# Performance work log

Hardware: AMD Instinct MI355X
Metric: run time of the kernel (lower is better)

## Reference

```python
import jax, jax.numpy as jnp
import numpy as np

B, S, H, NH = 2, 2048, 1024, 16
HD = H // NH
INV_NORM = 1.0 / float(np.sqrt(HD))
BETA = 1.0


def setup_inputs() -> dict:
    key = jax.random.key(0)
    ks = jax.random.split(key, 8)
    causal = ~jnp.tril(jnp.ones((S, S), dtype=bool))  # True = masked (future)
    return {
        "hidden_states": jax.random.normal(ks[0], (B, S, H), dtype=jnp.float32),
        "residual": jax.random.normal(ks[1], (B, S, H), dtype=jnp.float32),
        "alibi": jax.random.normal(ks[2], (B * NH, 1, S), dtype=jnp.float32) * 0.1,
        "attention_mask": jnp.broadcast_to(causal[None, None], (B, 1, S, S)),
        "W_qkv": jax.random.normal(ks[3], (3 * H, H), dtype=jnp.float32) * (1.0 / np.sqrt(H)),
        "b_qkv": jax.random.normal(ks[4], (3 * H,), dtype=jnp.float32) * 0.02,
        "W_d": jax.random.normal(ks[5], (H, H), dtype=jnp.float32) * (1.0 / np.sqrt(H)),
        "b_d": jax.random.normal(ks[6], (H,), dtype=jnp.float32) * 0.02,
    }


def reference(hidden_states, residual, alibi, attention_mask, W_qkv, b_qkv, W_d, b_d):
    b, s, h = hidden_states.shape
    # fused QKV projection, split per-head interleaved [B,S,NH,3,HD]
    fused = hidden_states @ W_qkv.T + b_qkv
    fused = fused.reshape(b, s, NH, 3, HD)
    q = jnp.transpose(fused[..., 0, :], (0, 2, 1, 3))  # [B,NH,S,HD]
    k = jnp.transpose(fused[..., 1, :], (0, 2, 1, 3))
    v = jnp.transpose(fused[..., 2, :], (0, 2, 1, 3))
    # baddbmm: beta*alibi + alpha * q @ k^T
    scores = BETA * alibi.reshape(b, NH, 1, s) + INV_NORM * jnp.einsum(
        "bhqd,bhkd->bhqk", q, k
    )  # [B,NH,S,S]
    neg_min = jnp.finfo(scores.dtype).min
    scores = jnp.where(attention_mask, neg_min, scores)
    probs = jax.nn.softmax(scores.astype(jnp.float32), axis=-1).astype(scores.dtype)
    ctx = jnp.einsum("bhqk,bhkd->bhqd", probs, v)  # [B,NH,S,HD]
    ctx = jnp.transpose(ctx, (0, 2, 1, 3)).reshape(b, s, h)  # merge heads
    out = ctx @ W_d.T + b_d
    return residual + out  # dropout p=0
```

## Files before the change

kernel.cpp:

```cpp
#include <hip/hip_runtime.h>
#include <stdint.h>

#define BATCH 2
#define SLEN 2048
#define HDIM 1024
#define NH 16
#define HD 64
#define NHEADS 32
#define M_ROWS 4096
#define N_QKV 3072

typedef float f32x4 __attribute__((ext_vector_type(4)));
typedef float f32x16 __attribute__((ext_vector_type(16)));
typedef short bf16x8 __attribute__((ext_vector_type(8)));

typedef __attribute__((address_space(1))) unsigned int GU32;
typedef __attribute__((address_space(3))) unsigned int LU32;

__device__ __forceinline__ void gld16(const void* g, void* l) {
  __builtin_amdgcn_global_load_lds((GU32*)g, (LU32*)l, 16, 0, 0);
}

__device__ __forceinline__ unsigned short f2bf(float x) {
  union { float f; unsigned int u; } v; v.f = x;
  unsigned int r = v.u + 0x7fffu + ((v.u >> 16) & 1u);
  return (unsigned short)(r >> 16);
}

__device__ __forceinline__ float fexp2(float x) {
  float r; asm("v_exp_f32 %0, %1" : "=v"(r) : "v"(x)); return r;
}
__device__ __forceinline__ unsigned cvtpk(float lo, float hi) {
  unsigned r; asm("v_cvt_pk_bf16_f32 %0, %1, %2" : "=v"(r) : "v"(lo), "v"(hi)); return r;
}

#define MFMA32(a, b, c) __builtin_amdgcn_mfma_f32_32x32x16_bf16(a, b, c, 0, 0, 0)
#define MFMA16(a, b, c) __builtin_amdgcn_mfma_f32_16x16x32_bf16(a, b, c, 0, 0, 0)
#define ZERO16 {0.f,0.f,0.f,0.f,0.f,0.f,0.f,0.f,0.f,0.f,0.f,0.f,0.f,0.f,0.f,0.f}

__global__ void __launch_bounds__(256) k_prep(
    const float* __restrict__ hidden, const float* __restrict__ wqkv,
    const float* __restrict__ wd,
    unsigned short* __restrict__ hb, unsigned short* __restrict__ wqkb,
    unsigned short* __restrict__ wdb) {
  int bid = blockIdx.x;
  const float* src;
  unsigned short* dst;
  int i;
  if (bid < 4096)      { src = hidden; dst = hb;   i = bid * 256 + threadIdx.x; }
  else if (bid < 7168) { src = wqkv;  dst = wqkb;  i = (bid - 4096) * 256 + threadIdx.x; }
  else                 { src = wd;    dst = wdb;   i = (bid - 7168) * 256 + threadIdx.x; }
  float4 v = ((const float4*)src)[i];
  ushort4 o;
  o.x = f2bf(v.x); o.y = f2bf(v.y); o.z = f2bf(v.z); o.w = f2bf(v.w);
  ((ushort4*)dst)[i] = o;
}

__global__ void __launch_bounds__(256) k_gemm_qkv(
    const unsigned short* __restrict__ A,
    const unsigned short* __restrict__ Bw,
    const float* __restrict__ bias,
    unsigned short* __restrict__ Qo,
    unsigned short* __restrict__ Ko,
    unsigned short* __restrict__ Vto) {
  __shared__ __align__(16) unsigned short Alds[128 * 32];
  __shared__ __align__(16) unsigned short Blds[128 * 32];
  const int tid = threadIdx.x;
  const int w = tid >> 6, lane = tid & 63;
  const int g = lane >> 4, l15 = lane & 15;
  const int wr = w >> 1, wc = w & 1;
  const int tm = blockIdx.x * 128, tn = blockIdx.y * 128;

  const f32x4 zero = {0.f, 0.f, 0.f, 0.f};
  f32x4 acc[4][4];
#pragma unroll
  for (int m = 0; m < 4; ++m)
#pragma unroll
    for (int n = 0; n < 4; ++n) acc[m][n] = zero;

  for (int k0 = 0; k0 < 1024; k0 += 32) {
    __syncthreads();
#pragma unroll
    for (int r = 0; r < 2; ++r) {
      int c = r * 256 + w * 64 + lane;
      int row = c >> 2, cc = c & 3;
      gld16(A + (size_t)(tm + row) * 1024 + k0 + cc * 8,
            (char*)Alds + (r * 256 + w * 64) * 16);
      gld16(Bw + (size_t)(tn + row) * 1024 + k0 + cc * 8,
            (char*)Blds + (r * 256 + w * 64) * 16);
    }
    __syncthreads();
    bf16x8 af[4], bfv[4];
#pragma unroll
    for (int m = 0; m < 4; ++m)
      af[m] = *(const bf16x8*)(Alds + (wr * 64 + m * 16 + l15) * 32 + g * 8);
#pragma unroll
    for (int n = 0; n < 4; ++n)
      bfv[n] = *(const bf16x8*)(Blds + (wc * 64 + n * 16 + l15) * 32 + g * 8);
#pragma unroll
    for (int m = 0; m < 4; ++m)
#pragma unroll
      for (int n = 0; n < 4; ++n)
        acc[m][n] = MFMA16(af[m], bfv[n], acc[m][n]);
  }

#pragma unroll
  for (int n = 0; n < 4; ++n) {
    int col = tn + wc * 64 + n * 16 + l15;
    float bv = bias[col];
    int c6 = col >> 6;
    int nh = c6 / 3;
    int which = c6 - nh * 3;
    int hd = col & 63;
#pragma unroll
    for (int m = 0; m < 4; ++m) {
      int row0 = tm + wr * 64 + m * 16 + g * 4;
      int b = row0 >> 11;
      int s0 = row0 & 2047;
      int head = b * NH + nh;
      if (which == 2) {
        ushort4 pk;
        pk.x = f2bf(acc[m][n][0] + bv);
        pk.y = f2bf(acc[m][n][1] + bv);
        pk.z = f2bf(acc[m][n][2] + bv);
        pk.w = f2bf(acc[m][n][3] + bv);
        *(ushort4*)(Vto + ((size_t)head * HD + hd) * SLEN + s0) = pk;
      } else {
        unsigned short* dst = (which == 0) ? Qo : Ko;
        size_t base = (size_t)head * SLEN * HD;
#pragma unroll
        for (int j = 0; j < 4; ++j)
          dst[base + (size_t)(s0 + j) * HD + hd] = f2bf(acc[m][n][j] + bv);
      }
    }
  }
}

__global__ void __launch_bounds__(256) k_gemm_out(
    const unsigned short* __restrict__ A,
    const unsigned short* __restrict__ Bw,
    const float* __restrict__ bias,
    const float* __restrict__ residual,
    float* __restrict__ out) {
  __shared__ __align__(16) unsigned short Alds[128 * 32];
  __shared__ __align__(16) unsigned short Blds[64 * 32];
  const int tid = threadIdx.x;
  const int w = tid >> 6, lane = tid & 63;
  const int g = lane >> 4, l15 = lane & 15;
  const int wr = w >> 1, wc = w & 1;
  const int tm = blockIdx.x * 128, tn = blockIdx.y * 64;

  const f32x4 zero = {0.f, 0.f, 0.f, 0.f};
  f32x4 acc[4][2];
#pragma unroll
  for (int m = 0; m < 4; ++m)
#pragma unroll
    for (int n = 0; n < 2; ++n) acc[m][n] = zero;

  for (int k0 = 0; k0 < 1024; k0 += 32) {
    __syncthreads();
#pragma unroll
    for (int r = 0; r < 2; ++r) {
      int c = r * 256 + tid;
      int row = c >> 2, cc = c & 3;
      gld16(A + (size_t)(tm + row) * 1024 + k0 + cc * 8,
            (char*)Alds + c * 16);
    }
    {
      int row = tid >> 2, cc = tid & 3;
      gld16(Bw + (size_t)(tn + row) * 1024 + k0 + cc * 8,
            (char*)Blds + tid * 16);
    }
    __syncthreads();
    bf16x8 af[4], bfv[2];
#pragma unroll
    for (int m = 0; m < 4; ++m)
      af[m] = *(const bf16x8*)(Alds + (wr * 64 + m * 16 + l15) * 32 + g * 8);
#pragma unroll
    for (int n = 0; n < 2; ++n)
      bfv[n] = *(const bf16x8*)(Blds + (wc * 32 + n * 16 + l15) * 32 + g * 8);
#pragma unroll
    for (int m = 0; m < 4; ++m)
#pragma unroll
      for (int n = 0; n < 2; ++n)
        acc[m][n] = MFMA16(af[m], bfv[n], acc[m][n]);
  }

#pragma unroll
  for (int n = 0; n < 2; ++n) {
    int col = tn + wc * 32 + n * 16 + l15;
    float bv = bias[col];
#pragma unroll
    for (int m = 0; m < 4; ++m) {
      int row0 = tm + wr * 64 + m * 16 + g * 4;
#pragma unroll
      for (int j = 0; j < 4; ++j) {
        size_t idx = (size_t)(row0 + j) * 1024 + col;
        out[idx] = acc[m][n][j] + bv + residual[idx];
      }
    }
  }
}

__global__ void __launch_bounds__(512, 4) k_attn(
    const unsigned short* __restrict__ Q,
    const unsigned short* __restrict__ K,
    const unsigned short* __restrict__ Vt,
    const float* __restrict__ alibi,
    unsigned short* __restrict__ ctx) {
  __shared__ __align__(16) char Lbuf[40960];
  unsigned short* KlB = (unsigned short*)Lbuf;
  unsigned short* VlB = (unsigned short*)(Lbuf + 16384);
  float* Al = (float*)(Lbuf + 32768);

  const int n = blockIdx.x;
  const int head = n & 31;
  const int t = n >> 5;
  const int bq = (t < 8) ? (15 - t) : (t - 8);
  const int tid = threadIdx.x;
  const int w = tid >> 6, lane = tid & 63;
  const int l31 = lane & 31, h = lane >> 5;
  const int rsw = l31 & 7;
  const int qsub = w & 3, par = w >> 2;
  const int qw = bq * 128 + qsub * 32;
  const int ksd = 4 * bq + qsub;

  const unsigned short* Qh = Q + (size_t)head * SLEN * HD;
  const unsigned short* Kh = K + (size_t)head * SLEN * HD;
  const unsigned short* Vh = Vt + (size_t)head * HD * SLEN;

  bf16x8 qr0, qr1, qr2, qr3;
  {
    const unsigned short* qp = Qh + (size_t)(qw + l31) * HD + h * 8;
    qr0 = *(const bf16x8*)(qp);
    qr1 = *(const bf16x8*)(qp + 16);
    qr2 = *(const bf16x8*)(qp + 32);
    qr3 = *(const bf16x8*)(qp + 48);
  }

  f32x16 ot0 = ZERO16, ot1 = ZERO16;
  float m_run = -1e30f, l_acc = 0.f;
  const float C1 = 0.18033688011f;

#define STAGE(nb, itt)                                                          \
  do {                                                                          \
    const int kb_ = (itt) * 64;                                                 \
    const int row_ = tid >> 3;                                                  \
    const int sw_ = ((tid & 7) ^ (row_ & 7)) * 8;                               \
    gld16(Kh + (size_t)(kb_ + row_) * HD + sw_, (char*)(KlB + (nb) * 4096) + tid * 16); \
    gld16(Vh + (size_t)row_ * SLEN + kb_ + sw_, (char*)(VlB + (nb) * 4096) + tid * 16); \
  } while (0)

  STAGE(0, 0);
  {
    float4 av = *(const float4*)(alibi + (size_t)head * SLEN + tid * 4);
    av.x *= 1.44269504f; av.y *= 1.44269504f;
    av.z *= 1.44269504f; av.w *= 1.44269504f;
    *(float4*)(Al + tid * 4) = av;
  }
  __syncthreads();
  int cur = 0;
  const int itmax = 2 * bq + 2;

  for (int it = 0; it < itmax; ++it) {
    if (it + 1 < itmax) STAGE(cur ^ 1, it + 1);
    const int ks = 2 * it + par;
    if (ks <= ksd) {
      const char* kbase = (const char*)(KlB + cur * 4096);
      const char* vbase = (const char*)(VlB + cur * 4096);

      f32x16 st = ZERO16;
      __builtin_amdgcn_s_setprio(1);
      {
        const char* kr = kbase + (par * 32 + l31) * 128;
        st = MFMA32(*(const bf16x8*)(kr + (((0 + h) ^ rsw) * 16)), qr0, st);
        st = MFMA32(*(const bf16x8*)(kr + (((2 + h) ^ rsw) * 16)), qr1, st);
        st = MFMA32(*(const bf16x8*)(kr + (((4 + h) ^ rsw) * 16)), qr2, st);
        st = MFMA32(*(const bf16x8*)(kr + (((6 + h) ^ rsw) * 16)), qr3, st);
      }
      __builtin_amdgcn_s_setprio(0);

      const float* ab = Al + ks * 32 + 4 * h;
      f32x4 alq0 = *(const f32x4*)(ab);
      f32x4 alq1 = *(const f32x4*)(ab + 8);
      f32x4 alq2 = *(const f32x4*)(ab + 16);
      f32x4 alq3 = *(const f32x4*)(ab + 24);

      float p[16];
#pragma unroll
      for (int i = 0; i < 4; ++i) {
        p[i]      = st[i]      * C1 + alq0[i];
        p[4 + i]  = st[4 + i]  * C1 + alq1[i];
        p[8 + i]  = st[8 + i]  * C1 + alq2[i];
        p[12 + i] = st[12 + i] * C1 + alq3[i];
      }
      if (ks == ksd) {
#pragma unroll
        for (int i = 0; i < 16; ++i) {
          int krow = (i & 3) + 8 * (i >> 2) + 4 * h;
          p[i] = (krow > l31) ? -1e30f : p[i];
        }
      }
      float x0 = fmaxf(fmaxf(p[0], p[1]), p[2]);
      float x1 = fmaxf(fmaxf(p[3], p[4]), p[5]);
      float x2 = fmaxf(fmaxf(p[6], p[7]), p[8]);
      float x3 = fmaxf(fmaxf(p[9], p[10]), p[11]);
      float x4 = fmaxf(fmaxf(p[12], p[13]), p[14]);
      float pm = fmaxf(fmaxf(fmaxf(x0, x1), x2), fmaxf(fmaxf(x3, x4), p[15]));
      pm = fmaxf(pm, __shfl_xor(pm, 32));
      if (!__all(pm <= m_run + 8.0f)) {
        float mnew = fmaxf(m_run, pm);
        float sc = fexp2(m_run - mnew);
        m_run = mnew;
        l_acc *= sc;
        ot0 *= sc;
        ot1 *= sc;
      }
      float e[16];
      float ss = 0.f;
#pragma unroll
      for (int i = 0; i < 16; ++i) { e[i] = fexp2(p[i] - m_run); ss += e[i]; }
      l_acc += ss;

      unsigned a0 = cvtpk(e[0], e[1]),   a1 = cvtpk(e[2], e[3]);
      unsigned a2 = cvtpk(e[4], e[5]),   a3 = cvtpk(e[6], e[7]);
      unsigned b0 = cvtpk(e[8], e[9]),   b1 = cvtpk(e[10], e[11]);
      unsigned b2 = cvtpk(e[12], e[13]), b3 = cvtpk(e[14], e[15]);
      unsigned t0 = h ? a0 : a2, t1 = h ? a1 : a3;
      unsigned t2 = h ? b0 : b2, t3 = h ? b1 : b3;
      unsigned r0 = __shfl_xor(t0, 32), r1 = __shfl_xor(t1, 32);
      unsigned r2 = __shfl_xor(t2, 32), r3 = __shfl_xor(t3, 32);
      union { unsigned u[4]; bf16x8 v; } P0, P1;
      P0.u[0] = h ? r0 : a0;  P0.u[1] = h ? r1 : a1;
      P0.u[2] = h ? a2 : r0;  P0.u[3] = h ? a3 : r1;
      P1.u[0] = h ? r2 : b0;  P1.u[1] = h ? r3 : b1;
      P1.u[2] = h ? b2 : r2;  P1.u[3] = h ? b3 : r3;

      __builtin_amdgcn_s_setprio(1);
      {
        const char* vr0 = vbase + l31 * 128;
        const char* vr1 = vbase + (32 + l31) * 128;
        bf16x8 vf;
        vf = *(const bf16x8*)(vr0 + (((4 * par + 0 + h) ^ rsw) * 16)); ot0 = MFMA32(vf, P0.v, ot0);
        vf = *(const bf16x8*)(vr0 + (((4 * par + 2 + h) ^ rsw) * 16)); ot0 = MFMA32(vf, P1.v, ot0);
        vf = *(const bf16x8*)(vr1 + (((4 * par + 0 + h) ^ rsw) * 16)); ot1 = MFMA32(vf, P0.v, ot1);
        vf = *(const bf16x8*)(vr1 + (((4 * par + 2 + h) ^ rsw) * 16)); ot1 = MFMA32(vf, P1.v, ot1);
      }
      __builtin_amdgcn_s_setprio(0);
    }
    __syncthreads();
    cur ^= 1;
  }
#undef STAGE

  float* Ob = (float*)Lbuf;
  float* Mb = (float*)(Lbuf + 32768);
  const int idx = qsub * 64 + lane;
  const int xs = idx & 7;
  float* op = Ob + (size_t)idx * 32;
  if (par == 1) {
#pragma unroll
    for (int c = 0; c < 4; ++c) {
      f32x4 t2 = {ot0[4 * c], ot0[4 * c + 1], ot0[4 * c + 2], ot0[4 * c + 3]};
      *(f32x4*)(op + ((c ^ xs) * 4)) = t2;
      f32x4 u = {ot1[4 * c], ot1[4 * c + 1], ot1[4 * c + 2], ot1[4 * c + 3]};
      *(f32x4*)(op + (((c + 4) ^ xs) * 4)) = u;
    }
    Mb[idx * 2] = m_run;
    Mb[idx * 2 + 1] = l_acc;
  }
  __syncthreads();
  if (par == 0) {
    float m1 = Mb[idx * 2], l1 = Mb[idx * 2 + 1];
    float mt = fmaxf(m_run, m1);
    float s0 = fexp2(m_run - mt), s1 = fexp2(m1 - mt);
    float lme = l_acc * s0 + l1 * s1;
    float ltot = lme + __shfl_xor(lme, 32);
    float inv = 1.0f / ltot;
#pragma unroll
    for (int c = 0; c < 4; ++c) {
      f32x4 t2 = *(const f32x4*)(op + ((c ^ xs) * 4));
      f32x4 u = *(const f32x4*)(op + (((c + 4) ^ xs) * 4));
#pragma unroll
      for (int j = 0; j < 4; ++j) {
        ot0[4 * c + j] = ot0[4 * c + j] * s0 + t2[j] * s1;
        ot1[4 * c + j] = ot1[4 * c + j] * s0 + u[j] * s1;
      }
    }
    const int b = head >> 4, nh = head & 15;
    unsigned short* cb = ctx + ((size_t)b * SLEN + qw + l31) * HDIM + nh * HD + 4 * h;
#pragma unroll
    for (int rg = 0; rg < 4; ++rg) {
      ushort4 o;
      o.x = f2bf(ot0[4 * rg + 0] * inv);
      o.y = f2bf(ot0[4 * rg + 1] * inv);
      o.z = f2bf(ot0[4 * rg + 2] * inv);
      o.w = f2bf(ot0[4 * rg + 3] * inv);
      *(ushort4*)(cb + 8 * rg) = o;
      o.x = f2bf(ot1[4 * rg + 0] * inv);
      o.y = f2bf(ot1[4 * rg + 1] * inv);
      o.z = f2bf(ot1[4 * rg + 2] * inv);
      o.w = f2bf(ot1[4 * rg + 3] * inv);
      *(ushort4*)(cb + 32 + 8 * rg) = o;
    }
  }
}

extern "C" void kernel_launch(void* const* d_in, const int* in_sizes, int n_in,
                              void* d_out, int out_size, void* d_ws, size_t ws_size,
                              hipStream_t stream) {
  const float* hidden   = (const float*)d_in[0];
  const float* residual = (const float*)d_in[1];
  const float* alibi    = (const float*)d_in[2];
  const float* W_qkv = (const float*)d_in[4];
  const float* b_qkv = (const float*)d_in[5];
  const float* W_d   = (const float*)d_in[6];
  const float* b_d   = (const float*)d_in[7];
  float* out = (float*)d_out;

  unsigned short* hb   = (unsigned short*)d_ws;
  unsigned short* wqkb = hb + (size_t)M_ROWS * HDIM;
  unsigned short* wdb  = wqkb + (size_t)N_QKV * HDIM;
  unsigned short* Qb   = wdb + (size_t)HDIM * HDIM;
  unsigned short* Kb   = Qb + (size_t)NHEADS * SLEN * HD;
  unsigned short* Vtb  = Kb + (size_t)NHEADS * SLEN * HD;
  unsigned short* ctxb = Vtb + (size_t)NHEADS * SLEN * HD;

  k_prep<<<dim3(8192), dim3(256), 0, stream>>>(hidden, W_qkv, W_d, hb, wqkb, wdb);
  k_gemm_qkv<<<dim3(32, 24), dim3(256), 0, stream>>>(hb, wqkb, b_qkv, Qb, Kb, Vtb);
  k_attn<<<dim3(512), dim3(512), 0, stream>>>(Qb, Kb, Vtb, alibi, ctxb);
  k_gemm_out<<<dim3(32, 16), dim3(256), 0, stream>>>(ctxb, wdb, b_d, residual, out);
}
```

Measured before the change: 103.0 us.

## Split attention blocks to 64 query rows with 4-way KV split and single-buffered 128-key tiles

The attention kernel now gives each block 64 query rows instead of 128 and launches twice as many blocks. Four warp groups now split the key range instead of two, followed by a two-stage LDS merge of the partial softmax states. Each iteration stages a 128-key K/V tile into a single buffer with a new 16-way V swizzle, in place of the double-buffered 64-key pipeline. The aim is more parallelism and better balance across the causal triangle. The cost is that load/compute overlap is lost, since a barrier now follows each stage, and the merge phase adds extra barriers.

Measured after the change: 104.5 us. Within noise of the previous version (+1.5%).

```diff
diff --git a/kernel.cpp b/kernel.cpp
--- a/kernel.cpp
+++ b/kernel.cpp
@@ -213,17 +213,17 @@
   unsigned short* VlB = (unsigned short*)(Lbuf + 16384);
   float* Al = (float*)(Lbuf + 32768);
 
-  const int n = blockIdx.x;
-  const int head = n & 31;
-  const int t = n >> 5;
-  const int bq = (t < 8) ? (15 - t) : (t - 8);
+  const int bid = blockIdx.x;
+  const int head = bid & 31;
+  const int bq = 31 - (bid >> 5);
   const int tid = threadIdx.x;
   const int w = tid >> 6, lane = tid & 63;
   const int l31 = lane & 31, h = lane >> 5;
   const int rsw = l31 & 7;
-  const int qsub = w & 3, par = w >> 2;
-  const int qw = bq * 128 + qsub * 32;
-  const int ksd = 4 * bq + qsub;
+  const int vsw = l31 & 15;
+  const int qsub = w & 1, par = w >> 1;
+  const int qw = bq * 64 + qsub * 32;
+  const int ksd = 2 * bq + qsub;
 
   const unsigned short* Qh = Q + (size_t)head * SLEN * HD;
   const unsigned short* Kh = K + (size_t)head * SLEN * HD;
@@ -242,37 +242,39 @@
   float m_run = -1e30f, l_acc = 0.f;
   const float C1 = 0.18033688011f;
 
-#define STAGE(nb, itt)                                                          \
-  do {                                                                          \
-    const int kb_ = (itt) * 64;                                                 \
-    const int row_ = tid >> 3;                                                  \
-    const int sw_ = ((tid & 7) ^ (row_ & 7)) * 8;                               \
-    gld16(Kh + (size_t)(kb_ + row_) * HD + sw_, (char*)(KlB + (nb) * 4096) + tid * 16); \
-    gld16(Vh + (size_t)row_ * SLEN + kb_ + sw_, (char*)(VlB + (nb) * 4096) + tid * 16); \
+#define STAGE(itt)                                                                  \
+  do {                                                                              \
+    const int kb_ = (itt) * 128;                                                    \
+    const int r0_ = tid >> 3, c0_ = tid & 7;                                        \
+    gld16(Kh + (size_t)(kb_ + r0_) * HD + ((c0_ ^ (r0_ & 7)) * 8),                  \
+          (char*)KlB + tid * 16);                                                   \
+    gld16(Kh + (size_t)(kb_ + 64 + r0_) * HD + ((c0_ ^ (r0_ & 7)) * 8),             \
+          (char*)KlB + (512 + tid) * 16);                                           \
+    const int vr0_ = tid >> 4, vc0_ = tid & 15;                                     \
+    gld16(Vh + (size_t)vr0_ * SLEN + kb_ + ((vc0_ ^ (vr0_ & 15)) * 8),              \
+          (char*)VlB + tid * 16);                                                   \
+    gld16(Vh + (size_t)(32 + vr0_) * SLEN + kb_ + ((vc0_ ^ (vr0_ & 15)) * 8),       \
+          (char*)VlB + (512 + tid) * 16);                                           \
   } while (0)
 
-  STAGE(0, 0);
   {
     float4 av = *(const float4*)(alibi + (size_t)head * SLEN + tid * 4);
     av.x *= 1.44269504f; av.y *= 1.44269504f;
     av.z *= 1.44269504f; av.w *= 1.44269504f;
     *(float4*)(Al + tid * 4) = av;
   }
-  __syncthreads();
-  int cur = 0;
-  const int itmax = 2 * bq + 2;
+
+  const int itmax = (2 * bq + 1) / 4 + 1;
 
   for (int it = 0; it < itmax; ++it) {
-    if (it + 1 < itmax) STAGE(cur ^ 1, it + 1);
-    const int ks = 2 * it + par;
+    STAGE(it);
+    __syncthreads();
+    const int ks = 4 * it + par;
     if (ks <= ksd) {
-      const char* kbase = (const char*)(KlB + cur * 4096);
-      const char* vbase = (const char*)(VlB + cur * 4096);
-
       f32x16 st = ZERO16;
       __builtin_amdgcn_s_setprio(1);
       {
-        const char* kr = kbase + (par * 32 + l31) * 128;
+        const char* kr = (const char*)KlB + (par * 32 + l31) * 128;
         st = MFMA32(*(const bf16x8*)(kr + (((0 + h) ^ rsw) * 16)), qr0, st);
         st = MFMA32(*(const bf16x8*)(kr + (((2 + h) ^ rsw) * 16)), qr1, st);
         st = MFMA32(*(const bf16x8*)(kr + (((4 + h) ^ rsw) * 16)), qr2, st);
@@ -338,55 +340,69 @@
 
       __builtin_amdgcn_s_setprio(1);
       {
-        const char* vr0 = vbase + l31 * 128;
-        const char* vr1 = vbase + (32 + l31) * 128;
+        const char* vr0 = (const char*)VlB + l31 * 256;
+        const char* vr1 = (const char*)VlB + (32 + l31) * 256;
         bf16x8 vf;
-        vf = *(const bf16x8*)(vr0 + (((4 * par + 0 + h) ^ rsw) * 16)); ot0 = MFMA32(vf, P0.v, ot0);
-        vf = *(const bf16x8*)(vr0 + (((4 * par + 2 + h) ^ rsw) * 16)); ot0 = MFMA32(vf, P1.v, ot0);
-        vf = *(const bf16x8*)(vr1 + (((4 * par + 0 + h) ^ rsw) * 16)); ot1 = MFMA32(vf, P0.v, ot1);
-        vf = *(const bf16x8*)(vr1 + (((4 * par + 2 + h) ^ rsw) * 16)); ot1 = MFMA32(vf, P1.v, ot1);
+        vf = *(const bf16x8*)(vr0 + (((4 * par + 0 + h) ^ vsw) * 16)); ot0 = MFMA32(vf, P0.v, ot0);
+        vf = *(const bf16x8*)(vr0 + (((4 * par + 2 + h) ^ vsw) * 16)); ot0 = MFMA32(vf, P1.v, ot0);
+        vf = *(const bf16x8*)(vr1 + (((4 * par + 0 + h) ^ vsw) * 16)); ot1 = MFMA32(vf, P0.v, ot1);
+        vf = *(const bf16x8*)(vr1 + (((4 * par + 2 + h) ^ vsw) * 16)); ot1 = MFMA32(vf, P1.v, ot1);
       }
       __builtin_amdgcn_s_setprio(0);
     }
     __syncthreads();
-    cur ^= 1;
   }
 #undef STAGE
 
   float* Ob = (float*)Lbuf;
   float* Mb = (float*)(Lbuf + 32768);
-  const int idx = qsub * 64 + lane;
-  const int xs = idx & 7;
-  float* op = Ob + (size_t)idx * 32;
-  if (par == 1) {
-#pragma unroll
-    for (int c = 0; c < 4; ++c) {
-      f32x4 t2 = {ot0[4 * c], ot0[4 * c + 1], ot0[4 * c + 2], ot0[4 * c + 3]};
-      *(f32x4*)(op + ((c ^ xs) * 4)) = t2;
-      f32x4 u = {ot1[4 * c], ot1[4 * c + 1], ot1[4 * c + 2], ot1[4 * c + 3]};
-      *(f32x4*)(op + (((c + 4) ^ xs) * 4)) = u;
-    }
-    Mb[idx * 2] = m_run;
-    Mb[idx * 2 + 1] = l_acc;
-  }
+  const int xs = lane & 7;
+
+#define WRITE_SLOT(slot)                                                   \
+  do {                                                                     \
+    float* op = Ob + ((size_t)(slot) * 64 + lane) * 32;                    \
+    _Pragma("unroll")                                                      \
+    for (int c = 0; c < 4; ++c) {                                          \
+      f32x4 t2 = {ot0[4*c], ot0[4*c+1], ot0[4*c+2], ot0[4*c+3]};           \
+      *(f32x4*)(op + ((c ^ xs) * 4)) = t2;                                 \
+      f32x4 u2 = {ot1[4*c], ot1[4*c+1], ot1[4*c+2], ot1[4*c+3]};           \
+      *(f32x4*)(op + (((c + 4) ^ xs) * 4)) = u2;                           \
+    }                                                                      \
+    Mb[((slot) * 64 + lane) * 2] = m_run;                                  \
+    Mb[((slot) * 64 + lane) * 2 + 1] = l_acc;                              \
+  } while (0)
+
+#define MERGE_SLOT(slot)                                                   \
+  do {                                                                     \
+    const float* op = Ob + ((size_t)(slot) * 64 + lane) * 32;              \
+    float m1 = Mb[((slot) * 64 + lane) * 2];                               \
+    float l1 = Mb[((slot) * 64 + lane) * 2 + 1];                           \
+    float mt = fmaxf(m_run, m1);                                           \
+    float s0 = fexp2(m_run - mt), s1 = fexp2(m1 - mt);                     \
+    m_run = mt;                                                            \
+    l_acc = l_acc * s0 + l1 * s1;                                          \
+    _Pragma("unroll")                                                      \
+    for (int c = 0; c < 4; ++c) {                                          \
+      f32x4 t2 = *(const f32x4*)(op + ((c ^ xs) * 4));                     \
+      f32x4 u2 = *(const f32x4*)(op + (((c + 4) ^ xs) * 4));               \
+      _Pragma("unroll")                                                    \
+      for (int j = 0; j < 4; ++j) {                                        \
+        ot0[4*c+j] = ot0[4*c+j] * s0 + t2[j] * s1;                         \
+        ot1[4*c+j] = ot1[4*c+j] * s0 + u2[j] * s1;                         \
+      }                                                                    \
+    }                                                                      \
+  } while (0)
+
+  if (par == 1 || par == 3) WRITE_SLOT(qsub * 2 + (par >> 1));
+  __syncthreads();
+  if (par == 0 || par == 2) MERGE_SLOT(qsub * 2 + (par >> 1));
+  __syncthreads();
+  if (par == 2) WRITE_SLOT(qsub * 2);
   __syncthreads();
   if (par == 0) {
-    float m1 = Mb[idx * 2], l1 = Mb[idx * 2 + 1];
-    float mt = fmaxf(m_run, m1);
-    float s0 = fexp2(m_run - mt), s1 = fexp2(m1 - mt);
-    float lme = l_acc * s0 + l1 * s1;
-    float ltot = lme + __shfl_xor(lme, 32);
+    MERGE_SLOT(qsub * 2);
+    float ltot = l_acc + __shfl_xor(l_acc, 32);
     float inv = 1.0f / ltot;
-#pragma unroll
-    for (int c = 0; c < 4; ++c) {
-      f32x4 t2 = *(const f32x4*)(op + ((c ^ xs) * 4));
-      f32x4 u = *(const f32x4*)(op + (((c + 4) ^ xs) * 4));
-#pragma unroll
-      for (int j = 0; j < 4; ++j) {
-        ot0[4 * c + j] = ot0[4 * c + j] * s0 + t2[j] * s1;
-        ot1[4 * c + j] = ot1[4 * c + j] * s0 + u[j] * s1;
-      }
-    }
     const int b = head >> 4, nh = head & 15;
     unsigned short* cb = ctx + ((size_t)b * SLEN + qw + l31) * HDIM + nh * HD + 4 * h;
 #pragma unroll
@@ -404,6 +420,8 @@
       *(ushort4*)(cb + 32 + 8 * rg) = o;
     }
   }
+#undef WRITE_SLOT
+#undef MERGE_SLOT
 }
 
 extern "C" void kernel_launch(void* const* d_in, const int* in_sizes, int n_in,
@@ -428,6 +446,6 @@
 
   k_prep<<<dim3(8192), dim3(256), 0, stream>>>(hidden, W_qkv, W_d, hb, wqkb, wdb);
   k_gemm_qkv<<<dim3(32, 24), dim3(256), 0, stream>>>(hb, wqkb, b_qkv, Qb, Kb, Vtb);
-  k_attn<<<dim3(512), dim3(512), 0, stream>>>(Qb, Kb, Vtb, alibi, ctxb);
+  k_attn<<<dim3(1024), dim3(512), 0, stream>>>(Qb, Kb, Vtb, alibi, ctxb);
   k_gemm_out<<<dim3(32, 16), dim3(256), 0, stream>>>(ctxb, wdb, b_d, residual, out);
 }
```

## Load K/V fragments directly from global memory in attention, drop LDS staging

Applied to the files above, without the earlier changes.

The attention kernel stops staging K and V tiles into shared memory with double-buffered global_load_lds and block-wide barriers. Each wave now reads its own K and V fragments straight from global memory (relying on L2/L1 for reuse) and iterates only its own key steps, with no per-iteration __syncthreads. The alibi prescale by log2(e) moves into the prep kernel, and attention reads the scaled alibi from global memory instead of LDS. This removes barrier coupling between waves, but loses the shared reuse of K/V across the four query sub-waves and exposes global load latency without explicit prefetch.

New measurement: 138.9 us. 34.9% more time.

```diff
diff --git a/kernel.cpp b/kernel.cpp
--- a/kernel.cpp
+++ b/kernel.cpp
@@ -40,16 +40,23 @@
 
 __global__ void __launch_bounds__(256) k_prep(
     const float* __restrict__ hidden, const float* __restrict__ wqkv,
-    const float* __restrict__ wd,
+    const float* __restrict__ wd, const float* __restrict__ alibi,
     unsigned short* __restrict__ hb, unsigned short* __restrict__ wqkb,
-    unsigned short* __restrict__ wdb) {
+    unsigned short* __restrict__ wdb, float* __restrict__ al2) {
   int bid = blockIdx.x;
   const float* src;
   unsigned short* dst;
   int i;
   if (bid < 4096)      { src = hidden; dst = hb;   i = bid * 256 + threadIdx.x; }
   else if (bid < 7168) { src = wqkv;  dst = wqkb;  i = (bid - 4096) * 256 + threadIdx.x; }
-  else                 { src = wd;    dst = wdb;   i = (bid - 7168) * 256 + threadIdx.x; }
+  else if (bid < 8192) { src = wd;    dst = wdb;   i = (bid - 7168) * 256 + threadIdx.x; }
+  else {
+    int j = (bid - 8192) * 256 + threadIdx.x;
+    float4 v = ((const float4*)alibi)[j];
+    v.x *= 1.44269504f; v.y *= 1.44269504f; v.z *= 1.44269504f; v.w *= 1.44269504f;
+    ((float4*)al2)[j] = v;
+    return;
+  }
   float4 v = ((const float4*)src)[i];
   ushort4 o;
   o.x = f2bf(v.x); o.y = f2bf(v.y); o.z = f2bf(v.z); o.w = f2bf(v.w);
@@ -206,12 +213,10 @@
     const unsigned short* __restrict__ Q,
     const unsigned short* __restrict__ K,
     const unsigned short* __restrict__ Vt,
-    const float* __restrict__ alibi,
+    const float* __restrict__ al2,
     unsigned short* __restrict__ ctx) {
-  __shared__ __align__(16) char Lbuf[40960];
-  unsigned short* KlB = (unsigned short*)Lbuf;
-  unsigned short* VlB = (unsigned short*)(Lbuf + 16384);
-  float* Al = (float*)(Lbuf + 32768);
+  __shared__ __align__(16) float Ob[256 * 32];
+  __shared__ __align__(16) float Mb[256 * 2];
 
   const int n = blockIdx.x;
   const int head = n & 31;
@@ -220,7 +225,6 @@
   const int tid = threadIdx.x;
   const int w = tid >> 6, lane = tid & 63;
   const int l31 = lane & 31, h = lane >> 5;
-  const int rsw = l31 & 7;
   const int qsub = w & 3, par = w >> 2;
   const int qw = bq * 128 + qsub * 32;
   const int ksd = 4 * bq + qsub;
@@ -228,6 +232,7 @@
   const unsigned short* Qh = Q + (size_t)head * SLEN * HD;
   const unsigned short* Kh = K + (size_t)head * SLEN * HD;
   const unsigned short* Vh = Vt + (size_t)head * HD * SLEN;
+  const float* alh = al2 + (size_t)head * SLEN;
 
   bf16x8 qr0, qr1, qr2, qr3;
   {
@@ -242,119 +247,98 @@
   float m_run = -1e30f, l_acc = 0.f;
   const float C1 = 0.18033688011f;
 
-#define STAGE(nb, itt)                                                          \
-  do {                                                                          \
-    const int kb_ = (itt) * 64;                                                 \
-    const int row_ = tid >> 3;                                                  \
-    const int sw_ = ((tid & 7) ^ (row_ & 7)) * 8;                               \
-    gld16(Kh + (size_t)(kb_ + row_) * HD + sw_, (char*)(KlB + (nb) * 4096) + tid * 16); \
-    gld16(Vh + (size_t)row_ * SLEN + kb_ + sw_, (char*)(VlB + (nb) * 4096) + tid * 16); \
-  } while (0)
-
-  STAGE(0, 0);
-  {
-    float4 av = *(const float4*)(alibi + (size_t)head * SLEN + tid * 4);
-    av.x *= 1.44269504f; av.y *= 1.44269504f;
-    av.z *= 1.44269504f; av.w *= 1.44269504f;
-    *(float4*)(Al + tid * 4) = av;
-  }
-  __syncthreads();
-  int cur = 0;
-  const int itmax = 2 * bq + 2;
-
-  for (int it = 0; it < itmax; ++it) {
-    if (it + 1 < itmax) STAGE(cur ^ 1, it + 1);
-    const int ks = 2 * it + par;
-    if (ks <= ksd) {
-      const char* kbase = (const char*)(KlB + cur * 4096);
-      const char* vbase = (const char*)(VlB + cur * 4096);
-
-      f32x16 st = ZERO16;
+  const unsigned short* krow = Kh + (size_t)l31 * HD + h * 8;
+  const unsigned short* vrow0 = Vh + (size_t)l31 * SLEN + h * 8;
+  const unsigned short* vrow1 = Vh + (size_t)(32 + l31) * SLEN + h * 8;
+
+  for (int ks = par; ks <= ksd; ks += 2) {
+    const unsigned short* kb = krow + (size_t)ks * 32 * HD;
+    f32x16 st = ZERO16;
+    {
+      bf16x8 kf0 = *(const bf16x8*)(kb);
+      bf16x8 kf1 = *(const bf16x8*)(kb + 16);
+      bf16x8 kf2 = *(const bf16x8*)(kb + 32);
+      bf16x8 kf3 = *(const bf16x8*)(kb + 48);
       __builtin_amdgcn_s_setprio(1);
-      {
-        const char* kr = kbase + (par * 32 + l31) * 128;
-        st = MFMA32(*(const bf16x8*)(kr + (((0 + h) ^ rsw) * 16)), qr0, st);
-        st = MFMA32(*(const bf16x8*)(kr + (((2 + h) ^ rsw) * 16)), qr1, st);
-        st = MFMA32(*(const bf16x8*)(kr + (((4 + h) ^ rsw) * 16)), qr2, st);
-        st = MFMA32(*(const bf16x8*)(kr + (((6 + h) ^ rsw) * 16)), qr3, st);
+      st = MFMA32(kf0, qr0, st);
+      st = MFMA32(kf1, qr1, st);
+      st = MFMA32(kf2, qr2, st);
+      st = MFMA32(kf3, qr3, st);
+      __builtin_amdgcn_s_setprio(0);
+    }
+
+    const float* ab = alh + ks * 32 + 4 * h;
+    f32x4 alq0 = *(const f32x4*)(ab);
+    f32x4 alq1 = *(const f32x4*)(ab + 8);
+    f32x4 alq2 = *(const f32x4*)(ab + 16);
+    f32x4 alq3 = *(const f32x4*)(ab + 24);
+
+    float p[16];
+#pragma unroll
+    for (int i = 0; i < 4; ++i) {
+      p[i]      = st[i]      * C1 + alq0[i];
+      p[4 + i]  = st[4 + i]  * C1 + alq1[i];
+      p[8 + i]  = st[8 + i]  * C1 + alq2[i];
+      p[12 + i] = st[12 + i] * C1 + alq3[i];
+    }
+    if (ks == ksd) {
+#pragma unroll
+      for (int i = 0; i < 16; ++i) {
+        int krw = (i & 3) + 8 * (i >> 2) + 4 * h;
+        p[i] = (krw > l31) ? -1e30f : p[i];
       }
+    }
+    float x0 = fmaxf(fmaxf(p[0], p[1]), p[2]);
+    float x1 = fmaxf(fmaxf(p[3], p[4]), p[5]);
+    float x2 = fmaxf(fmaxf(p[6], p[7]), p[8]);
+    float x3 = fmaxf(fmaxf(p[9], p[10]), p[11]);
+    float x4 = fmaxf(fmaxf(p[12], p[13]), p[14]);
+    float pm = fmaxf(fmaxf(fmaxf(x0, x1), x2), fmaxf(fmaxf(x3, x4), p[15]));
+    pm = fmaxf(pm, __shfl_xor(pm, 32));
+    if (!__all(pm <= m_run + 8.0f)) {
+      float mnew = fmaxf(m_run, pm);
+      float sc = fexp2(m_run - mnew);
+      m_run = mnew;
+      l_acc *= sc;
+      ot0 *= sc;
+      ot1 *= sc;
+    }
+    float e[16];
+    float ss = 0.f;
+#pragma unroll
+    for (int i = 0; i < 16; ++i) { e[i] = fexp2(p[i] - m_run); ss += e[i]; }
+    l_acc += ss;
+
+    unsigned a0 = cvtpk(e[0], e[1]),   a1 = cvtpk(e[2], e[3]);
+    unsigned a2 = cvtpk(e[4], e[5]),   a3 = cvtpk(e[6], e[7]);
+    unsigned b0 = cvtpk(e[8], e[9]),   b1 = cvtpk(e[10], e[11]);
+    unsigned b2 = cvtpk(e[12], e[13]), b3 = cvtpk(e[14], e[15]);
+    unsigned t0 = h ? a0 : a2, t1 = h ? a1 : a3;
+    unsigned t2 = h ? b0 : b2, t3 = h ? b1 : b3;
+    unsigned r0 = __shfl_xor(t0, 32), r1 = __shfl_xor(t1, 32);
+    unsigned r2 = __shfl_xor(t2, 32), r3 = __shfl_xor(t3, 32);
+    union { unsigned u[4]; bf16x8 v; } P0, P1;
+    P0.u[0] = h ? r0 : a0;  P0.u[1] = h ? r1 : a1;
+    P0.u[2] = h ? a2 : r0;  P0.u[3] = h ? a3 : r1;
+    P1.u[0] = h ? r2 : b0;  P1.u[1] = h ? r3 : b1;
+    P1.u[2] = h ? b2 : r2;  P1.u[3] = h ? b3 : r3;
+
+    {
+      const unsigned short* v0 = vrow0 + ks * 32;
+      const unsigned short* v1 = vrow1 + ks * 32;
+      bf16x8 vf00 = *(const bf16x8*)(v0);
+      bf16x8 vf01 = *(const bf16x8*)(v0 + 16);
+      bf16x8 vf10 = *(const bf16x8*)(v1);
+      bf16x8 vf11 = *(const bf16x8*)(v1 + 16);
+      __builtin_amdgcn_s_setprio(1);
+      ot0 = MFMA32(vf00, P0.v, ot0);
+      ot0 = MFMA32(vf01, P1.v, ot0);
+      ot1 = MFMA32(vf10, P0.v, ot1);
+      ot1 = MFMA32(vf11, P1.v, ot1);
       __builtin_amdgcn_s_setprio(0);
-
-      const float* ab = Al + ks * 32 + 4 * h;
-      f32x4 alq0 = *(const f32x4*)(ab);
-      f32x4 alq1 = *(const f32x4*)(ab + 8);
-      f32x4 alq2 = *(const f32x4*)(ab + 16);
-      f32x4 alq3 = *(const f32x4*)(ab + 24);
-
-      float p[16];
-#pragma unroll
-      for (int i = 0; i < 4; ++i) {
-        p[i]      = st[i]      * C1 + alq0[i];
-        p[4 + i]  = st[4 + i]  * C1 + alq1[i];
-        p[8 + i]  = st[8 + i]  * C1 + alq2[i];
-        p[12 + i] = st[12 + i] * C1 + alq3[i];
-      }
-      if (ks == ksd) {
-#pragma unroll
-        for (int i = 0; i < 16; ++i) {
-          int krow = (i & 3) + 8 * (i >> 2) + 4 * h;
-          p[i] = (krow > l31) ? -1e30f : p[i];
-        }
-      }
-      float x0 = fmaxf(fmaxf(p[0], p[1]), p[2]);
-      float x1 = fmaxf(fmaxf(p[3], p[4]), p[5]);
-      float x2 = fmaxf(fmaxf(p[6], p[7]), p[8]);
-      float x3 = fmaxf(fmaxf(p[9], p[10]), p[11]);
-      float x4 = fmaxf(fmaxf(p[12], p[13]), p[14]);
-      float pm = fmaxf(fmaxf(fmaxf(x0, x1), x2), fmaxf(fmaxf(x3, x4), p[15]));
-      pm = fmaxf(pm, __shfl_xor(pm, 32));
-      if (!__all(pm <= m_run + 8.0f)) {
-        float mnew = fmaxf(m_run, pm);
-        float sc = fexp2(m_run - mnew);
-        m_run = mnew;
-        l_acc *= sc;
-        ot0 *= sc;
-        ot1 *= sc;
-      }
-      float e[16];
-      float ss = 0.f;
-#pragma unroll
-      for (int i = 0; i < 16; ++i) { e[i] = fexp2(p[i] - m_run); ss += e[i]; }
-      l_acc += ss;
-
-      unsigned a0 = cvtpk(e[0], e[1]),   a1 = cvtpk(e[2], e[3]);
-      unsigned a2 = cvtpk(e[4], e[5]),   a3 = cvtpk(e[6], e[7]);
-      unsigned b0 = cvtpk(e[8], e[9]),   b1 = cvtpk(e[10], e[11]);
-      unsigned b2 = cvtpk(e[12], e[13]), b3 = cvtpk(e[14], e[15]);
-      unsigned t0 = h ? a0 : a2, t1 = h ? a1 : a3;
-      unsigned t2 = h ? b0 : b2, t3 = h ? b1 : b3;
-      unsigned r0 = __shfl_xor(t0, 32), r1 = __shfl_xor(t1, 32);
-      unsigned r2 = __shfl_xor(t2, 32), r3 = __shfl_xor(t3, 32);
-      union { unsigned u[4]; bf16x8 v; } P0, P1;
-      P0.u[0] = h ? r0 : a0;  P0.u[1] = h ? r1 : a1;
-      P0.u[2] = h ? a2 : r0;  P0.u[3] = h ? a3 : r1;
-      P1.u[0] = h ? r2 : b0;  P1.u[1] = h ? r3 : b1;
-      P1.u[2] = h ? b2 : r2;  P1.u[3] = h ? b3 : r3;
-
-      __builtin_amdgcn_s_setprio(1);
-      {
-        const char* vr0 = vbase + l31 * 128;
-        const char* vr1 = vbase + (32 + l31) * 128;
-        bf16x8 vf;
-        vf = *(const bf16x8*)(vr0 + (((4 * par + 0 + h) ^ rsw) * 16)); ot0 = MFMA32(vf, P0.v, ot0);
-        vf = *(const bf16x8*)(vr0 + (((4 * par + 2 + h) ^ rsw) * 16)); ot0 = MFMA32(vf, P1.v, ot0);
-        vf = *(const bf16x8*)(vr1 + (((4 * par + 0 + h) ^ rsw) * 16)); ot1 = MFMA32(vf, P0.v, ot1);
-        vf = *(const bf16x8*)(vr1 + (((4 * par + 2 + h) ^ rsw) * 16)); ot1 = MFMA32(vf, P1.v, ot1);
-      }
-      __builtin_amdgcn_s_setprio(0);
-    }
-    __syncthreads();
-    cur ^= 1;
-  }
-#undef STAGE
-
-  float* Ob = (float*)Lbuf;
-  float* Mb = (float*)(Lbuf + 32768);
+    }
+  }
+
   const int idx = qsub * 64 + lane;
   const int xs = idx & 7;
   float* op = Ob + (size_t)idx * 32;
@@ -425,9 +409,10 @@
   unsigned short* Kb   = Qb + (size_t)NHEADS * SLEN * HD;
   unsigned short* Vtb  = Kb + (size_t)NHEADS * SLEN * HD;
   unsigned short* ctxb = Vtb + (size_t)NHEADS * SLEN * HD;
-
-  k_prep<<<dim3(8192), dim3(256), 0, stream>>>(hidden, W_qkv, W_d, hb, wqkb, wdb);
+  float* al2b = (float*)(ctxb + (size_t)M_ROWS * HDIM);
+
+  k_prep<<<dim3(8256), dim3(256), 0, stream>>>(hidden, W_qkv, W_d, alibi, hb, wqkb, wdb, al2b);
   k_gemm_qkv<<<dim3(32, 24), dim3(256), 0, stream>>>(hb, wqkb, b_qkv, Qb, Kb, Vtb);
-  k_attn<<<dim3(512), dim3(512), 0, stream>>>(Qb, Kb, Vtb, alibi, ctxb);
+  k_attn<<<dim3(512), dim3(512), 0, stream>>>(Qb, Kb, Vtb, al2b, ctxb);
   k_gemm_out<<<dim3(32, 16), dim3(256), 0, stream>>>(ctxb, wdb, b_d, residual, out);
 }
```

## Process both key sub-blocks per warp in attention, dropping the split-K merge

Applied to the files above, without the earlier changes.

The attention kernel now runs 4 warps per block instead of 8. Each warp handles both 32-key halves of every 64-key tile, where before two warp groups each took one half and merged partial softmax state through LDS at the end. This removes the final merge, its extra barrier and the LDS round trip, and halves threads per block. In exchange each warp does twice the serial work per tile, with fewer warps to hide latency and more registers live.

Result: slower. 172.0 us (+67.0%).

```diff
diff --git a/kernel.cpp b/kernel.cpp
--- a/kernel.cpp
+++ b/kernel.cpp
@@ -202,7 +202,7 @@
   }
 }
 
-__global__ void __launch_bounds__(512, 4) k_attn(
+__global__ void __launch_bounds__(256, 4) k_attn(
     const unsigned short* __restrict__ Q,
     const unsigned short* __restrict__ K,
     const unsigned short* __restrict__ Vt,
@@ -221,9 +221,8 @@
   const int w = tid >> 6, lane = tid & 63;
   const int l31 = lane & 31, h = lane >> 5;
   const int rsw = l31 & 7;
-  const int qsub = w & 3, par = w >> 2;
-  const int qw = bq * 128 + qsub * 32;
-  const int ksd = 4 * bq + qsub;
+  const int qw = bq * 128 + w * 32;
+  const int ksd = 4 * bq + w;
 
   const unsigned short* Qh = Q + (size_t)head * SLEN * HD;
   const unsigned short* Kh = K + (size_t)head * SLEN * HD;
@@ -245,18 +244,24 @@
 #define STAGE(nb, itt)                                                          \
   do {                                                                          \
     const int kb_ = (itt) * 64;                                                 \
-    const int row_ = tid >> 3;                                                  \
-    const int sw_ = ((tid & 7) ^ (row_ & 7)) * 8;                               \
-    gld16(Kh + (size_t)(kb_ + row_) * HD + sw_, (char*)(KlB + (nb) * 4096) + tid * 16); \
-    gld16(Vh + (size_t)row_ * SLEN + kb_ + sw_, (char*)(VlB + (nb) * 4096) + tid * 16); \
+    const int i0_ = tid, i1_ = tid + 256;                                       \
+    const int r0_ = i0_ >> 3, s0_ = ((i0_ & 7) ^ (r0_ & 7)) * 8;                \
+    const int r1_ = i1_ >> 3, s1_ = ((i1_ & 7) ^ (r1_ & 7)) * 8;                \
+    gld16(Kh + (size_t)(kb_ + r0_) * HD + s0_, (char*)(KlB + (nb) * 4096) + i0_ * 16); \
+    gld16(Kh + (size_t)(kb_ + r1_) * HD + s1_, (char*)(KlB + (nb) * 4096) + i1_ * 16); \
+    gld16(Vh + (size_t)r0_ * SLEN + kb_ + s0_, (char*)(VlB + (nb) * 4096) + i0_ * 16); \
+    gld16(Vh + (size_t)r1_ * SLEN + kb_ + s1_, (char*)(VlB + (nb) * 4096) + i1_ * 16); \
   } while (0)
 
   STAGE(0, 0);
   {
-    float4 av = *(const float4*)(alibi + (size_t)head * SLEN + tid * 4);
-    av.x *= 1.44269504f; av.y *= 1.44269504f;
-    av.z *= 1.44269504f; av.w *= 1.44269504f;
-    *(float4*)(Al + tid * 4) = av;
+    const float* as = alibi + (size_t)head * SLEN;
+    float4 a0 = *(const float4*)(as + tid * 4);
+    float4 a1 = *(const float4*)(as + 1024 + tid * 4);
+    a0.x *= 1.44269504f; a0.y *= 1.44269504f; a0.z *= 1.44269504f; a0.w *= 1.44269504f;
+    a1.x *= 1.44269504f; a1.y *= 1.44269504f; a1.z *= 1.44269504f; a1.w *= 1.44269504f;
+    *(float4*)(Al + tid * 4) = a0;
+    *(float4*)(Al + 1024 + tid * 4) = a1;
   }
   __syncthreads();
   int cur = 0;
@@ -264,49 +269,87 @@
 
   for (int it = 0; it < itmax; ++it) {
     if (it + 1 < itmax) STAGE(cur ^ 1, it + 1);
-    const int ks = 2 * it + par;
-    if (ks <= ksd) {
+    const int ks0 = 2 * it, ks1 = 2 * it + 1;
+    const bool h0 = (ks0 <= ksd), h1 = (ks1 <= ksd);
+    if (h0) {
       const char* kbase = (const char*)(KlB + cur * 4096);
       const char* vbase = (const char*)(VlB + cur * 4096);
 
-      f32x16 st = ZERO16;
+      f32x16 st0 = ZERO16, st1 = ZERO16;
       __builtin_amdgcn_s_setprio(1);
       {
-        const char* kr = kbase + (par * 32 + l31) * 128;
-        st = MFMA32(*(const bf16x8*)(kr + (((0 + h) ^ rsw) * 16)), qr0, st);
-        st = MFMA32(*(const bf16x8*)(kr + (((2 + h) ^ rsw) * 16)), qr1, st);
-        st = MFMA32(*(const bf16x8*)(kr + (((4 + h) ^ rsw) * 16)), qr2, st);
-        st = MFMA32(*(const bf16x8*)(kr + (((6 + h) ^ rsw) * 16)), qr3, st);
+        const char* kr = kbase + l31 * 128;
+        st0 = MFMA32(*(const bf16x8*)(kr + (((0 + h) ^ rsw) * 16)), qr0, st0);
+        st0 = MFMA32(*(const bf16x8*)(kr + (((2 + h) ^ rsw) * 16)), qr1, st0);
+        st0 = MFMA32(*(const bf16x8*)(kr + (((4 + h) ^ rsw) * 16)), qr2, st0);
+        st0 = MFMA32(*(const bf16x8*)(kr + (((6 + h) ^ rsw) * 16)), qr3, st0);
+      }
+      if (h1) {
+        const char* kr = kbase + (32 + l31) * 128;
+        st1 = MFMA32(*(const bf16x8*)(kr + (((0 + h) ^ rsw) * 16)), qr0, st1);
+        st1 = MFMA32(*(const bf16x8*)(kr + (((2 + h) ^ rsw) * 16)), qr1, st1);
+        st1 = MFMA32(*(const bf16x8*)(kr + (((4 + h) ^ rsw) * 16)), qr2, st1);
+        st1 = MFMA32(*(const bf16x8*)(kr + (((6 + h) ^ rsw) * 16)), qr3, st1);
       }
       __builtin_amdgcn_s_setprio(0);
 
-      const float* ab = Al + ks * 32 + 4 * h;
-      f32x4 alq0 = *(const f32x4*)(ab);
-      f32x4 alq1 = *(const f32x4*)(ab + 8);
-      f32x4 alq2 = *(const f32x4*)(ab + 16);
-      f32x4 alq3 = *(const f32x4*)(ab + 24);
-
-      float p[16];
-#pragma unroll
-      for (int i = 0; i < 4; ++i) {
-        p[i]      = st[i]      * C1 + alq0[i];
-        p[4 + i]  = st[4 + i]  * C1 + alq1[i];
-        p[8 + i]  = st[8 + i]  * C1 + alq2[i];
-        p[12 + i] = st[12 + i] * C1 + alq3[i];
-      }
-      if (ks == ksd) {
+      float p0[16], p1[16];
+      {
+        const float* ab = Al + ks0 * 32 + 4 * h;
+        f32x4 a0 = *(const f32x4*)(ab);
+        f32x4 a1 = *(const f32x4*)(ab + 8);
+        f32x4 a2 = *(const f32x4*)(ab + 16);
+        f32x4 a3 = *(const f32x4*)(ab + 24);
+#pragma unroll
+        for (int i = 0; i < 4; ++i) {
+          p0[i]      = st0[i]      * C1 + a0[i];
+          p0[4 + i]  = st0[4 + i]  * C1 + a1[i];
+          p0[8 + i]  = st0[8 + i]  * C1 + a2[i];
+          p0[12 + i] = st0[12 + i] * C1 + a3[i];
+        }
+      }
+      if (h1) {
+        const float* ab = Al + ks1 * 32 + 4 * h;
+        f32x4 a0 = *(const f32x4*)(ab);
+        f32x4 a1 = *(const f32x4*)(ab + 8);
+        f32x4 a2 = *(const f32x4*)(ab + 16);
+        f32x4 a3 = *(const f32x4*)(ab + 24);
+#pragma unroll
+        for (int i = 0; i < 4; ++i) {
+          p1[i]      = st1[i]      * C1 + a0[i];
+          p1[4 + i]  = st1[4 + i]  * C1 + a1[i];
+          p1[8 + i]  = st1[8 + i]  * C1 + a2[i];
+          p1[12 + i] = st1[12 + i] * C1 + a3[i];
+        }
+      }
+      if (ks0 == ksd) {
 #pragma unroll
         for (int i = 0; i < 16; ++i) {
-          int krow = (i & 3) + 8 * (i >> 2) + 4 * h;
-          p[i] = (krow > l31) ? -1e30f : p[i];
+          int krw = (i & 3) + 8 * (i >> 2) + 4 * h;
+          p0[i] = (krw > l31) ? -1e30f : p0[i];
         }
       }
-      float x0 = fmaxf(fmaxf(p[0], p[1]), p[2]);
-      float x1 = fmaxf(fmaxf(p[3], p[4]), p[5]);
-      float x2 = fmaxf(fmaxf(p[6], p[7]), p[8]);
-      float x3 = fmaxf(fmaxf(p[9], p[10]), p[11]);
-      float x4 = fmaxf(fmaxf(p[12], p[13]), p[14]);
-      float pm = fmaxf(fmaxf(fmaxf(x0, x1), x2), fmaxf(fmaxf(x3, x4), p[15]));
+      if (h1 && ks1 == ksd) {
+#pragma unroll
+        for (int i = 0; i < 16; ++i) {
+          int krw = (i & 3) + 8 * (i >> 2) + 4 * h;
+          p1[i] = (krw > l31) ? -1e30f : p1[i];
+        }
+      }
+      float x0 = fmaxf(fmaxf(p0[0], p0[1]), p0[2]);
+      float x1 = fmaxf(fmaxf(p0[3], p0[4]), p0[5]);
+      float x2 = fmaxf(fmaxf(p0[6], p0[7]), p0[8]);
+      float x3 = fmaxf(fmaxf(p0[9], p0[10]), p0[11]);
+      float x4 = fmaxf(fmaxf(p0[12], p0[13]), p0[14]);
+      float pm = fmaxf(fmaxf(fmaxf(x0, x1), x2), fmaxf(fmaxf(x3, x4), p0[15]));
+      if (h1) {
+        float y0 = fmaxf(fmaxf(p1[0], p1[1]), p1[2]);
+        float y1 = fmaxf(fmaxf(p1[3], p1[4]), p1[5]);
+        float y2 = fmaxf(fmaxf(p1[6], p1[7]), p1[8]);
+        float y3 = fmaxf(fmaxf(p1[9], p1[10]), p1[11]);
+        float y4 = fmaxf(fmaxf(p1[12], p1[13]), p1[14]);
+        pm = fmaxf(pm, fmaxf(fmaxf(fmaxf(y0, y1), y2), fmaxf(fmaxf(y3, y4), p1[15])));
+      }
       pm = fmaxf(pm, __shfl_xor(pm, 32));
       if (!__all(pm <= m_run + 8.0f)) {
         float mnew = fmaxf(m_run, pm);
@@ -316,35 +359,61 @@
         ot0 *= sc;
         ot1 *= sc;
       }
-      float e[16];
+      float e0[16], e1[16];
       float ss = 0.f;
 #pragma unroll
-      for (int i = 0; i < 16; ++i) { e[i] = fexp2(p[i] - m_run); ss += e[i]; }
+      for (int i = 0; i < 16; ++i) { e0[i] = fexp2(p0[i] - m_run); ss += e0[i]; }
+      if (h1) {
+#pragma unroll
+        for (int i = 0; i < 16; ++i) { e1[i] = fexp2(p1[i] - m_run); ss += e1[i]; }
+      }
       l_acc += ss;
 
-      unsigned a0 = cvtpk(e[0], e[1]),   a1 = cvtpk(e[2], e[3]);
-      unsigned a2 = cvtpk(e[4], e[5]),   a3 = cvtpk(e[6], e[7]);
-      unsigned b0 = cvtpk(e[8], e[9]),   b1 = cvtpk(e[10], e[11]);
-      unsigned b2 = cvtpk(e[12], e[13]), b3 = cvtpk(e[14], e[15]);
-      unsigned t0 = h ? a0 : a2, t1 = h ? a1 : a3;
-      unsigned t2 = h ? b0 : b2, t3 = h ? b1 : b3;
-      unsigned r0 = __shfl_xor(t0, 32), r1 = __shfl_xor(t1, 32);
-      unsigned r2 = __shfl_xor(t2, 32), r3 = __shfl_xor(t3, 32);
-      union { unsigned u[4]; bf16x8 v; } P0, P1;
-      P0.u[0] = h ? r0 : a0;  P0.u[1] = h ? r1 : a1;
-      P0.u[2] = h ? a2 : r0;  P0.u[3] = h ? a3 : r1;
-      P1.u[0] = h ? r2 : b0;  P1.u[1] = h ? r3 : b1;
-      P1.u[2] = h ? b2 : r2;  P1.u[3] = h ? b3 : r3;
+      union { unsigned u[4]; bf16x8 v; } P0, P1, P2, P3;
+      {
+        unsigned a0 = cvtpk(e0[0], e0[1]),   a1 = cvtpk(e0[2], e0[3]);
+        unsigned a2 = cvtpk(e0[4], e0[5]),   a3 = cvtpk(e0[6], e0[7]);
+        unsigned b0 = cvtpk(e0[8], e0[9]),   b1 = cvtpk(e0[10], e0[11]);
+        unsigned b2 = cvtpk(e0[12], e0[13]), b3 = cvtpk(e0[14], e0[15]);
+        unsigned t0 = h ? a0 : a2, t1 = h ? a1 : a3;
+        unsigned t2 = h ? b0 : b2, t3 = h ? b1 : b3;
+        unsigned r0 = __shfl_xor(t0, 32), r1 = __shfl_xor(t1, 32);
+        unsigned r2 = __shfl_xor(t2, 32), r3 = __shfl_xor(t3, 32);
+        P0.u[0] = h ? r0 : a0;  P0.u[1] = h ? r1 : a1;
+        P0.u[2] = h ? a2 : r0;  P0.u[3] = h ? a3 : r1;
+        P1.u[0] = h ? r2 : b0;  P1.u[1] = h ? r3 : b1;
+        P1.u[2] = h ? b2 : r2;  P1.u[3] = h ? b3 : r3;
+      }
+      if (h1) {
+        unsigned a0 = cvtpk(e1[0], e1[1]),   a1 = cvtpk(e1[2], e1[3]);
+        unsigned a2 = cvtpk(e1[4], e1[5]),   a3 = cvtpk(e1[6], e1[7]);
+        unsigned b0 = cvtpk(e1[8], e1[9]),   b1 = cvtpk(e1[10], e1[11]);
+        unsigned b2 = cvtpk(e1[12], e1[13]), b3 = cvtpk(e1[14], e1[15]);
+        unsigned t0 = h ? a0 : a2, t1 = h ? a1 : a3;
+        unsigned t2 = h ? b0 : b2, t3 = h ? b1 : b3;
+        unsigned r0 = __shfl_xor(t0, 32), r1 = __shfl_xor(t1, 32);
+        unsigned r2 = __shfl_xor(t2, 32), r3 = __shfl_xor(t3, 32);
+        P2.u[0] = h ? r0 : a0;  P2.u[1] = h ? r1 : a1;
+        P2.u[2] = h ? a2 : r0;  P2.u[3] = h ? a3 : r1;
+        P3.u[0] = h ? r2 : b0;  P3.u[1] = h ? r3 : b1;
+        P3.u[2] = h ? b2 : r2;  P3.u[3] = h ? b3 : r3;
+      }
 
       __builtin_amdgcn_s_setprio(1);
       {
         const char* vr0 = vbase + l31 * 128;
         const char* vr1 = vbase + (32 + l31) * 128;
         bf16x8 vf;
-        vf = *(const bf16x8*)(vr0 + (((4 * par + 0 + h) ^ rsw) * 16)); ot0 = MFMA32(vf, P0.v, ot0);
-        vf = *(const bf16x8*)(vr0 + (((4 * par + 2 + h) ^ rsw) * 16)); ot0 = MFMA32(vf, P1.v, ot0);
-        vf = *(const bf16x8*)(vr1 + (((4 * par + 0 + h) ^ rsw) * 16)); ot1 = MFMA32(vf, P0.v, ot1);
-        vf = *(const bf16x8*)(vr1 + (((4 * par + 2 + h) ^ rsw) * 16)); ot1 = MFMA32(vf, P1.v, ot1);
+        vf = *(const bf16x8*)(vr0 + (((0 + h) ^ rsw) * 16)); ot0 = MFMA32(vf, P0.v, ot0);
+        vf = *(const bf16x8*)(vr0 + (((2 + h) ^ rsw) * 16)); ot0 = MFMA32(vf, P1.v, ot0);
+        vf = *(const bf16x8*)(vr1 + (((0 + h) ^ rsw) * 16)); ot1 = MFMA32(vf, P0.v, ot1);
+        vf = *(const bf16x8*)(vr1 + (((2 + h) ^ rsw) * 16)); ot1 = MFMA32(vf, P1.v, ot1);
+        if (h1) {
+          vf = *(const bf16x8*)(vr0 + (((4 + h) ^ rsw) * 16)); ot0 = MFMA32(vf, P2.v, ot0);
+          vf = *(const bf16x8*)(vr0 + (((6 + h) ^ rsw) * 16)); ot0 = MFMA32(vf, P3.v, ot0);
+          vf = *(const bf16x8*)(vr1 + (((4 + h) ^ rsw) * 16)); ot1 = MFMA32(vf, P2.v, ot1);
+          vf = *(const bf16x8*)(vr1 + (((6 + h) ^ rsw) * 16)); ot1 = MFMA32(vf, P3.v, ot1);
+        }
       }
       __builtin_amdgcn_s_setprio(0);
     }
@@ -353,56 +422,23 @@
   }
 #undef STAGE
 
-  float* Ob = (float*)Lbuf;
-  float* Mb = (float*)(Lbuf + 32768);
-  const int idx = qsub * 64 + lane;
-  const int xs = idx & 7;
-  float* op = Ob + (size_t)idx * 32;
-  if (par == 1) {
-#pragma unroll
-    for (int c = 0; c < 4; ++c) {
-      f32x4 t2 = {ot0[4 * c], ot0[4 * c + 1], ot0[4 * c + 2], ot0[4 * c + 3]};
-      *(f32x4*)(op + ((c ^ xs) * 4)) = t2;
-      f32x4 u = {ot1[4 * c], ot1[4 * c + 1], ot1[4 * c + 2], ot1[4 * c + 3]};
-      *(f32x4*)(op + (((c + 4) ^ xs) * 4)) = u;
-    }
-    Mb[idx * 2] = m_run;
-    Mb[idx * 2 + 1] = l_acc;
-  }
-  __syncthreads();
-  if (par == 0) {
-    float m1 = Mb[idx * 2], l1 = Mb[idx * 2 + 1];
-    float mt = fmaxf(m_run, m1);
-    float s0 = fexp2(m_run - mt), s1 = fexp2(m1 - mt);
-    float lme = l_acc * s0 + l1 * s1;
-    float ltot = lme + __shfl_xor(lme, 32);
-    float inv = 1.0f / ltot;
-#pragma unroll
-    for (int c = 0; c < 4; ++c) {
-      f32x4 t2 = *(const f32x4*)(op + ((c ^ xs) * 4));
-      f32x4 u = *(const f32x4*)(op + (((c + 4) ^ xs) * 4));
-#pragma unroll
-      for (int j = 0; j < 4; ++j) {
-        ot0[4 * c + j] = ot0[4 * c + j] * s0 + t2[j] * s1;
-        ot1[4 * c + j] = ot1[4 * c + j] * s0 + u[j] * s1;
-      }
-    }
-    const int b = head >> 4, nh = head & 15;
-    unsigned short* cb = ctx + ((size_t)b * SLEN + qw + l31) * HDIM + nh * HD + 4 * h;
-#pragma unroll
-    for (int rg = 0; rg < 4; ++rg) {
-      ushort4 o;
-      o.x = f2bf(ot0[4 * rg + 0] * inv);
-      o.y = f2bf(ot0[4 * rg + 1] * inv);
-      o.z = f2bf(ot0[4 * rg + 2] * inv);
-      o.w = f2bf(ot0[4 * rg + 3] * inv);
-      *(ushort4*)(cb + 8 * rg) = o;
-      o.x = f2bf(ot1[4 * rg + 0] * inv);
-      o.y = f2bf(ot1[4 * rg + 1] * inv);
-      o.z = f2bf(ot1[4 * rg + 2] * inv);
-      o.w = f2bf(ot1[4 * rg + 3] * inv);
-      *(ushort4*)(cb + 32 + 8 * rg) = o;
-    }
+  float ltot = l_acc + __shfl_xor(l_acc, 32);
+  float inv = 1.0f / ltot;
+  const int b = head >> 4, nh = head & 15;
+  unsigned short* cb = ctx + ((size_t)b * SLEN + qw + l31) * HDIM + nh * HD + 4 * h;
+#pragma unroll
+  for (int rg = 0; rg < 4; ++rg) {
+    ushort4 o;
+    o.x = f2bf(ot0[4 * rg + 0] * inv);
+    o.y = f2bf(ot0[4 * rg + 1] * inv);
+    o.z = f2bf(ot0[4 * rg + 2] * inv);
+    o.w = f2bf(ot0[4 * rg + 3] * inv);
+    *(ushort4*)(cb + 8 * rg) = o;
+    o.x = f2bf(ot1[4 * rg + 0] * inv);
+    o.y = f2bf(ot1[4 * rg + 1] * inv);
+    o.z = f2bf(ot1[4 * rg + 2] * inv);
+    o.w = f2bf(ot1[4 * rg + 3] * inv);
+    *(ushort4*)(cb + 32 + 8 * rg) = o;
   }
 }
 
@@ -428,6 +464,6 @@
 
   k_prep<<<dim3(8192), dim3(256), 0, stream>>>(hidden, W_qkv, W_d, hb, wqkb, wdb);
   k_gemm_qkv<<<dim3(32, 24), dim3(256), 0, stream>>>(hb, wqkb, b_qkv, Qb, Kb, Vtb);
-  k_attn<<<dim3(512), dim3(512), 0, stream>>>(Qb, Kb, Vtb, alibi, ctxb);
+  k_attn<<<dim3(512), dim3(256), 0, stream>>>(Qb, Kb, Vtb, alibi, ctxb);
   k_gemm_out<<<dim3(32, 16), dim3(256), 0, stream>>>(ctxb, wdb, b_d, residual, out);
 }
```
